# Kernel tuning notes

Measured on AMD Instinct MI355X. Metric: run time of the kernel, lower is better.

The kernel has to match this reference:

```python
import jax, jax.numpy as jnp
import numpy as np

N_QUBITS = 10
N_LAYERS = 2
B = 4096
D_IN = 512
D_OUT = 256


def _apply_1q(state, gate, wire, n):
    # state: (B, 2**n) complex64; gate: (2,2) shared or (B,2,2) batched
    b = state.shape[0]
    left, right = 2 ** wire, 2 ** (n - wire - 1)
    s = state.reshape(b, left, 2, right)
    if gate.ndim == 3:
        s = jnp.einsum('bij,bljr->blir', gate, s)
    else:
        s = jnp.einsum('ij,bljr->blir', gate, s)
    return s.reshape(b, 2 ** n)


def _apply_cnot(state, c, t, n):
    # CNOT(control=c, target=t): flip target axis on the control=1 slice
    b = state.shape[0]
    a, d = (c, t) if c < t else (t, c)
    s = state.reshape(b, 2 ** a, 2, 2 ** (d - a - 1), 2, 2 ** (n - d - 1))
    if c < t:
        s = s.at[:, :, 1].set(jnp.flip(s[:, :, 1], axis=3))
    else:
        s = s.at[:, :, :, :, 1].set(jnp.flip(s[:, :, :, :, 1], axis=2))
    return s.reshape(b, 2 ** n)


def _quantum_circuit(angles, qweights):
    # AngleEmbedding (RX) + StronglyEntanglingLayers (Rot + ring CNOTs), expval(PauliZ_i)
    b, n = angles.shape
    n_layers = qweights.shape[0]
    state = jnp.zeros((b, 2 ** n), jnp.complex64).at[:, 0].set(1.0)
    # AngleEmbedding default rotation='X': RX(angle_i) on wire i
    half = 0.5 * angles
    cx = jnp.cos(half).astype(jnp.complex64)
    sx = ((-1j) * jnp.sin(half)).astype(jnp.complex64)
    for i in range(n):
        gate = jnp.stack([jnp.stack([cx[:, i], sx[:, i]], -1),
                          jnp.stack([sx[:, i], cx[:, i]], -1)], -2)  # (B,2,2)
        state = _apply_1q(state, gate, i, n)
    for l in range(n_layers):
        phi, theta, omega = qweights[l, :, 0], qweights[l, :, 1], qweights[l, :, 2]
        ct = jnp.cos(0.5 * theta).astype(jnp.complex64)
        st = jnp.sin(0.5 * theta).astype(jnp.complex64)
        epo = jnp.exp(-0.5j * (phi + omega)).astype(jnp.complex64)
        epm = jnp.exp(-0.5j * (phi - omega)).astype(jnp.complex64)
        # Rot(phi,theta,omega) = RZ(omega) RY(theta) RZ(phi)
        gates = jnp.stack([jnp.stack([epo * ct, -jnp.conj(epm) * st], -1),
                           jnp.stack([epm * st, jnp.conj(epo) * ct], -1)], -2)  # (n,2,2)
        for i in range(n):
            state = _apply_1q(state, gates[i], i, n)
        if n > 1:
            r = (l % (n - 1)) + 1  # default StronglyEntanglingLayers range
            for i in range(n):
                state = _apply_cnot(state, i, (i + r) % n, n)
    probs = state.real ** 2 + state.imag ** 2  # (B, 2**n)
    k = np.arange(2 ** n)
    # wire 0 is the most-significant bit; z_i = +1 for bit 0, -1 for bit 1
    zmat = (1 - 2 * ((k[None, :] >> (n - 1 - np.arange(n))[:, None]) & 1)).astype(np.float32)
    return probs @ zmat.T  # (B, n)


def setup_inputs() -> dict:
    key = jax.random.key(0)
    ks = jax.random.split(key, 6)
    x = jax.random.normal(ks[0], (B, D_IN), jnp.float32)
    W_in = jax.random.normal(ks[1], (D_IN, N_QUBITS), jnp.float32) / np.float32(np.sqrt(D_IN))
    b_in = jnp.zeros((N_QUBITS,), jnp.float32)
    qweights = jax.random.uniform(ks[2], (N_LAYERS, N_QUBITS, 3), jnp.float32, 0.0, 2.0 * np.pi)
    W1 = jax.random.normal(ks[3], (N_QUBITS, 64), jnp.float32) / np.float32(np.sqrt(N_QUBITS))
    b1 = jnp.zeros((64,), jnp.float32)
    W2 = jax.random.normal(ks[4], (64, D_OUT), jnp.float32) / np.float32(8.0)
    b2 = jnp.zeros((D_OUT,), jnp.float32)
    return {'x': x, 'W_in': W_in, 'b_in': b_in, 'qweights': qweights,
            'W1': W1, 'b1': b1, 'W2': W2, 'b2': b2}


def reference(x, W_in, b_in, qweights, W1, b1, W2, b2):
    angles = x @ W_in + b_in          # input projection -> rotation angles
    z = _quantum_circuit(angles, qweights)  # (B, n_qubits) PauliZ expvals
    h = jax.nn.relu(z @ W1 + b1)
    return jnp.tanh(h @ W2 + b2)
```

## Files before the change

kernel.cpp:

```cpp
#include <hip/hip_runtime.h>
#include <math.h>

#define NQ 10

__device__ __forceinline__ void write_term(int u, const float abc[NQ][3],
                                           uint2* __restrict__ terms) {
    const int lane = u & 255, s = u >> 8;
    int q = -1, g0 = 0;
    if      (lane < 32)  { q = 8; g0 = 0;   }
    else if (lane < 64)  { q = 9; g0 = 32;  }
    else if (lane < 96)  { q = 0; g0 = 64;  }
    else if (lane < 128) { q = 1; g0 = 96;  }
    else if (lane < 160) { q = 6; g0 = 128; }
    else if (lane < 192) { q = 7; g0 = 160; }
    else if (lane < 200) { q = 4; g0 = 192; }
    else if (lane < 208) { q = 5; g0 = 200; }
    else if (lane < 216) { q = 2; g0 = 208; }
    else if (lane < 224) { q = 3; g0 = 216; }
    if (q < 0) { terms[u] = make_uint2(0u, 0u); return; }
    const int tau = (lane - g0) * 8 + s;

    int m = 1 << q;
    for (int ii = NQ - 1; ii >= 0; --ii) {
        int tt = (ii + 2) % NQ;
        if ((m >> tt) & 1) m ^= 1 << ii;
    }
    const int Lp = __popc(m);
    int cnt = 1;
    for (int k = 0; k < Lp; ++k) cnt *= 3;
    if (tau >= cnt) { terms[u] = make_uint2(0u, 0u); return; }

    int rem = tau;
    unsigned xm = 0, zm = 0;
    float coef = 1.f;
    for (int i = 0; i < NQ; ++i) {
        if ((m >> i) & 1) {
            int d = rem % 3; rem /= 3;
            coef *= abc[i][d];
            if (d == 0)      { xm |= 1u << i; }
            else if (d == 1) { xm |= 1u << i; zm |= 1u << i; }
            else             { zm |= 1u << i; }
        }
    }
    unsigned sgn = 0;
    for (int i = NQ - 1; i >= 0; --i) {
        int c = i, tt = (i + 1) % NQ;
        unsigned xc = (xm >> c) & 1u, zt = (zm >> tt) & 1u;
        unsigned xt = (xm >> tt) & 1u, zc = (zm >> c) & 1u;
        sgn ^= xc & zt & (xt ^ zc ^ 1u);
        xm ^= xc << tt;
        zm ^= zt << c;
    }
    if (sgn) coef = -coef;

    unsigned nib = 0;
    for (int p = 0; p < 5; ++p) {
        unsigned c0 = ((xm >> (2 * p)) & 1u) | (((zm >> (2 * p)) & 1u) << 1);
        unsigned c1 = ((xm >> (2 * p + 1)) & 1u) | (((zm >> (2 * p + 1)) & 1u) << 1);
        nib |= (c0 | (c1 << 2)) << (4 * p);
    }
    terms[u] = make_uint2(nib, __float_as_uint(coef));
}

__global__ __launch_bounds__(256) void qse_setup(const float* __restrict__ qw,
                                                 uint2* __restrict__ terms,
                                                 float* __restrict__ Rmat) {
    __shared__ float abc[NQ][3];
    const int t = threadIdx.x;
    const int b = blockIdx.x;
    if (t < NQ) {
        if (b == 0) {
            float phi = qw[t * 3 + 0], th = qw[t * 3 + 1], om = qw[t * 3 + 2];
            float st_, ct;  sincosf(0.5f * th, &st_, &ct);
            float spo, cpo; sincosf(0.5f * (phi + om), &spo, &cpo);
            float spm, cpm; sincosf(0.5f * (phi - om), &spm, &cpm);
            Rmat[t * 8 + 0] =  cpo * ct;  Rmat[t * 8 + 1] = -spo * ct;
            Rmat[t * 8 + 2] = -cpm * st_; Rmat[t * 8 + 3] = -spm * st_;
            Rmat[t * 8 + 4] =  cpm * st_; Rmat[t * 8 + 5] = -spm * st_;
            Rmat[t * 8 + 6] =  cpo * ct;  Rmat[t * 8 + 7] =  spo * ct;
        }
        {
            float phi = qw[30 + t * 3 + 0], th = qw[30 + t * 3 + 1], om = qw[30 + t * 3 + 2];
            float st_, ct;  sincosf(0.5f * th, &st_, &ct);
            float spo, cpo; sincosf(0.5f * (phi + om), &spo, &cpo);
            float spm, cpm; sincosf(0.5f * (phi - om), &spm, &cpm);
            float2 G00 = make_float2(cpo * ct, -spo * ct);
            float2 G01 = make_float2(-cpm * st_, -spm * st_);
            float2 G10 = make_float2(cpm * st_, -spm * st_);
            float2 G11 = make_float2(cpo * ct, spo * ct);
            float re = G00.x * G01.x + G00.y * G01.y - (G10.x * G11.x + G10.y * G11.y);
            float im = G00.x * G01.y - G00.y * G01.x - (G10.x * G11.y - G10.y * G11.x);
            float A00 = G00.x * G00.x + G00.y * G00.y - (G10.x * G10.x + G10.y * G10.y);
            float A11 = G01.x * G01.x + G01.y * G01.y - (G11.x * G11.x + G11.y * G11.y);
            abc[t][0] = re;
            abc[t][1] = -im;
            abc[t][2] = 0.5f * (A00 - A11);
        }
    }
    __syncthreads();
    write_term(b * 256 + t, abc, terms);
}

__device__ __forceinline__ float fast_tanh(float v) {
    float e = __expf(2.f * v);
    return 1.f - 2.f / (e + 1.f);
}

__global__ __launch_bounds__(256) void qse_mega(
    const float* __restrict__ x,
    const float* __restrict__ W_in,
    const float* __restrict__ b_in,
    const float* __restrict__ W1,
    const float* __restrict__ b1,
    const float* __restrict__ W2,
    const float* __restrict__ b2,
    const uint2* __restrict__ terms,
    const float* __restrict__ Rmat,
    float* __restrict__ out)
{
    __shared__ float angsh[4][NQ];
    __shared__ float E2d[4][5][32];
    __shared__ float zsh[4][NQ];
    __shared__ float hsh[4][64];

    const int t = threadIdx.x;
    const int lane = t & 63;
    const int wv = t >> 6;
    const int row0 = blockIdx.x * 4;

    uint2 tm[8];
    #pragma unroll
    for (int s = 0; s < 8; ++s) tm[s] = terms[s * 256 + t];

    {
        float acc[NQ];
        #pragma unroll
        for (int q = 0; q < NQ; ++q) acc[q] = 0.f;
        const float4* xr4 = (const float4*)(x + (size_t)(row0 + wv) * 512);
        #pragma unroll
        for (int k = 0; k < 2; ++k) {
            const int j4 = lane + 64 * k;
            const float4 xv = xr4[j4];
            const float* wr = W_in + (4 * j4) * NQ;
            #pragma unroll
            for (int h = 0; h < 5; ++h) {
                float2 w2 = ((const float2*)wr)[h];
                acc[2*h]   = fmaf(xv.x, w2.x, acc[2*h]);
                acc[2*h+1] = fmaf(xv.x, w2.y, acc[2*h+1]);
            }
            #pragma unroll
            for (int h = 0; h < 5; ++h) {
                float2 w2 = ((const float2*)(wr + NQ))[h];
                acc[2*h]   = fmaf(xv.y, w2.x, acc[2*h]);
                acc[2*h+1] = fmaf(xv.y, w2.y, acc[2*h+1]);
            }
            #pragma unroll
            for (int h = 0; h < 5; ++h) {
                float2 w2 = ((const float2*)(wr + 2 * NQ))[h];
                acc[2*h]   = fmaf(xv.z, w2.x, acc[2*h]);
                acc[2*h+1] = fmaf(xv.z, w2.y, acc[2*h+1]);
            }
            #pragma unroll
            for (int h = 0; h < 5; ++h) {
                float2 w2 = ((const float2*)(wr + 3 * NQ))[h];
                acc[2*h]   = fmaf(xv.w, w2.x, acc[2*h]);
                acc[2*h+1] = fmaf(xv.w, w2.y, acc[2*h+1]);
            }
        }
        #pragma unroll
        for (int off = 32; off > 0; off >>= 1) {
            #pragma unroll
            for (int q = 0; q < NQ; ++q) acc[q] += __shfl_xor(acc[q], off);
        }
        if (lane == 0) {
            #pragma unroll
            for (int q = 0; q < NQ; ++q) angsh[wv][q] = acc[q] + b_in[q];
        }
    }
    __syncthreads();

    if (t < 80) {
        const int rr = t / 20, rem = t % 20, p = rem >> 2, c1 = rem & 3;
        const int i0 = 2 * p, i1 = i0 + 1;
        float a0 = angsh[rr][i0];
        float a1 = angsh[rr][i1];
        float s0, c0f, s1, c1f;
        sincosf(0.5f * a0, &s0, &c0f);
        sincosf(0.5f * a1, &s1, &c1f);
        const float* Rp0 = Rmat + i0 * 8;
        const float* Rp1 = Rmat + i1 * 8;
        float2 u0 = make_float2(fmaf(Rp0[0], c0f, s0 * Rp0[3]), fmaf(Rp0[1], c0f, -s0 * Rp0[2]));
        float2 u1 = make_float2(fmaf(Rp0[4], c0f, s0 * Rp0[7]), fmaf(Rp0[5], c0f, -s0 * Rp0[6]));
        float ex0 = 2.f * (u0.x * u1.x + u0.y * u1.y);
        float ey0 = 2.f * (u0.x * u1.y - u0.y * u1.x);
        float ez0 = u0.x * u0.x + u0.y * u0.y - u1.x * u1.x - u1.y * u1.y;
        float2 v0 = make_float2(fmaf(Rp1[0], c1f, s1 * Rp1[3]), fmaf(Rp1[1], c1f, -s1 * Rp1[2]));
        float2 v1 = make_float2(fmaf(Rp1[4], c1f, s1 * Rp1[7]), fmaf(Rp1[5], c1f, -s1 * Rp1[6]));
        float ex1 = 2.f * (v0.x * v1.x + v0.y * v1.y);
        float ey1 = 2.f * (v0.x * v1.y - v0.y * v1.x);
        float ez1 = v0.x * v0.x + v0.y * v0.y - v1.x * v1.x - v1.y * v1.y;
        float e1 = (c1 == 0) ? 1.f : (c1 == 1) ? ex1 : (c1 == 2) ? ez1 : ey1;
        float e0arr[4] = {1.f, ex0, ez0, ey0};
        #pragma unroll
        for (int cc = 0; cc < 4; ++cc) {
            float v = e0arr[cc] * e1;
            int idx = cc | (c1 << 2);
            E2d[rr][p][2 * idx]     = v;
            E2d[rr][p][2 * idx + 1] = v;
        }
    }
    __syncthreads();

    float accR[4] = {0.f, 0.f, 0.f, 0.f};
    {
        const float* E2p = &E2d[0][0][0] + (t & 1);
        #pragma unroll
        for (int s = 0; s < 8; ++s) {
            const float cf = __uint_as_float(tm[s].y);
            const unsigned nib = tm[s].x;
            #pragma unroll
            for (int rr = 0; rr < 4; ++rr) {
                float pr = cf;
                #pragma unroll
                for (int p = 0; p < 5; ++p)
                    pr *= E2p[(rr * 5 + p) * 32 + 2 * ((nib >> (4 * p)) & 15u)];
                accR[rr] += pr;
            }
        }
    }
    #pragma unroll
    for (int rr = 0; rr < 4; ++rr) {
        accR[rr] += __shfl_xor(accR[rr], 1);
        accR[rr] += __shfl_xor(accR[rr], 2);
        accR[rr] += __shfl_xor(accR[rr], 4);
    }
    if (t < 192) {
        #pragma unroll
        for (int rr = 0; rr < 4; ++rr) {
            accR[rr] += __shfl_xor(accR[rr], 8);
            accR[rr] += __shfl_xor(accR[rr], 16);
        }
    }
    {
        int qx = -1;
        if      (t == 0)   qx = 8;
        else if (t == 32)  qx = 9;
        else if (t == 64)  qx = 0;
        else if (t == 96)  qx = 1;
        else if (t == 128) qx = 6;
        else if (t == 160) qx = 7;
        else if (t == 192) qx = 4;
        else if (t == 200) qx = 5;
        else if (t == 208) qx = 2;
        else if (t == 216) qx = 3;
        if (qx >= 0) {
            #pragma unroll
            for (int rr = 0; rr < 4; ++rr) zsh[rr][qx] = accR[rr];
        }
    }
    __syncthreads();

    {
        const int rr = t >> 6, c = t & 63;
        float a = b1[c];
        #pragma unroll
        for (int i = 0; i < NQ; ++i) a = fmaf(zsh[rr][i], W1[i * 64 + c], a);
        hsh[rr][c] = fmaxf(a, 0.f);
    }
    __syncthreads();

    {
        float oacc[4];
        const float bb = b2[t];
        #pragma unroll
        for (int rr = 0; rr < 4; ++rr) oacc[rr] = bb;
        for (int j4 = 0; j4 < 16; ++j4) {
            const float w0 = W2[(4 * j4 + 0) * 256 + t];
            const float w1 = W2[(4 * j4 + 1) * 256 + t];
            const float w2 = W2[(4 * j4 + 2) * 256 + t];
            const float w3 = W2[(4 * j4 + 3) * 256 + t];
            #pragma unroll
            for (int rr = 0; rr < 4; ++rr) {
                float4 hv = *(const float4*)&hsh[rr][4 * j4];
                oacc[rr] = fmaf(hv.x, w0, oacc[rr]);
                oacc[rr] = fmaf(hv.y, w1, oacc[rr]);
                oacc[rr] = fmaf(hv.z, w2, oacc[rr]);
                oacc[rr] = fmaf(hv.w, w3, oacc[rr]);
            }
        }
        #pragma unroll
        for (int rr = 0; rr < 4; ++rr)
            out[(size_t)(row0 + rr) * 256 + t] = fast_tanh(oacc[rr]);
    }
}

extern "C" void kernel_launch(void* const* d_in, const int* in_sizes, int n_in,
                              void* d_out, int out_size, void* d_ws, size_t ws_size,
                              hipStream_t stream) {
    const float* x    = (const float*)d_in[0];
    const float* W_in = (const float*)d_in[1];
    const float* b_in = (const float*)d_in[2];
    const float* qw   = (const float*)d_in[3];
    const float* W1   = (const float*)d_in[4];
    const float* b1   = (const float*)d_in[5];
    const float* W2   = (const float*)d_in[6];
    const float* b2   = (const float*)d_in[7];
    float* out = (float*)d_out;

    uint2* terms = (uint2*)d_ws;
    float* Rmat  = (float*)((char*)d_ws + 16384);

    qse_setup<<<8, 256, 0, stream>>>(qw, terms, Rmat);
    qse_mega<<<1024, 256, 0, stream>>>(x, W_in, b_in, W1, b1, W2, b2,
                                       (const uint2*)terms, (const float*)Rmat, out);
}
```

Measured before the change: 87.52 us.

## Precompute 4-qubit expectation tables and trim per-wave term slots

Replaces the five per-pair lookups per Pauli term with two 256-entry 4-qubit product tables plus one pair table, built in shared memory per row. This cuts shared loads and multiplies in the term-summation loop. It also sizes the number of term slots per wave to the actual term counts, so waves 1-3 skip the empty iterations. In exchange it adds a table-building pass and an extra barrier, and the non-uniform per-wave loop counts could cost some register or branch overhead.

New measurement: 84.92 us. 3.0% less time.

```diff
diff --git a/kernel.cpp b/kernel.cpp
--- a/kernel.cpp
+++ b/kernel.cpp
@@ -6,6 +6,8 @@
 __device__ __forceinline__ void write_term(int u, const float abc[NQ][3],
                                            uint2* __restrict__ terms) {
     const int lane = u & 255, s = u >> 8;
+    const int wvv = lane >> 6;
+    const int nsl = (wvv == 0) ? 8 : ((wvv == 3) ? 4 : 3);
     int q = -1, g0 = 0;
     if      (lane < 32)  { q = 8; g0 = 0;   }
     else if (lane < 64)  { q = 9; g0 = 32;  }
@@ -17,8 +19,8 @@
     else if (lane < 208) { q = 5; g0 = 200; }
     else if (lane < 216) { q = 2; g0 = 208; }
     else if (lane < 224) { q = 3; g0 = 216; }
-    if (q < 0) { terms[u] = make_uint2(0u, 0u); return; }
-    const int tau = (lane - g0) * 8 + s;
+    if (q < 0 || s >= nsl) { terms[u] = make_uint2(0u, 0u); return; }
+    const int tau = (lane - g0) * nsl + s;
 
     int m = 1 << q;
     for (int ii = NQ - 1; ii >= 0; --ii) {
@@ -53,13 +55,12 @@
     }
     if (sgn) coef = -coef;
 
-    unsigned nib = 0;
-    for (int p = 0; p < 5; ++p) {
-        unsigned c0 = ((xm >> (2 * p)) & 1u) | (((zm >> (2 * p)) & 1u) << 1);
-        unsigned c1 = ((xm >> (2 * p + 1)) & 1u) | (((zm >> (2 * p + 1)) & 1u) << 1);
-        nib |= (c0 | (c1 << 2)) << (4 * p);
-    }
-    terms[u] = make_uint2(nib, __float_as_uint(coef));
+    unsigned w = 0;
+    for (int i = 0; i < NQ; ++i) {
+        unsigned code = ((xm >> i) & 1u) | (((zm >> i) & 1u) << 1);
+        w |= code << (2 * i);
+    }
+    terms[u] = make_uint2(w, __float_as_uint(coef));
 }
 
 __global__ __launch_bounds__(256) void qse_setup(const float* __restrict__ qw,
@@ -119,7 +120,9 @@
     float* __restrict__ out)
 {
     __shared__ float angsh[4][NQ];
-    __shared__ float E2d[4][5][32];
+    __shared__ float E2tmp[4][5][16];
+    __shared__ float E4d[4][2][256];
+    __shared__ float E2P[4][32];
     __shared__ float zsh[4][NQ];
     __shared__ float hsh[4][64];
 
@@ -127,10 +130,12 @@
     const int lane = t & 63;
     const int wv = t >> 6;
     const int row0 = blockIdx.x * 4;
+    const int nsl = (wv == 0) ? 8 : ((wv == 3) ? 4 : 3);
 
     uint2 tm[8];
     #pragma unroll
-    for (int s = 0; s < 8; ++s) tm[s] = terms[s * 256 + t];
+    for (int s = 0; s < 8; ++s)
+        tm[s] = (s < nsl) ? terms[s * 256 + t] : make_uint2(0u, 0u);
 
     {
         float acc[NQ];
@@ -205,26 +210,38 @@
         for (int cc = 0; cc < 4; ++cc) {
             float v = e0arr[cc] * e1;
             int idx = cc | (c1 << 2);
-            E2d[rr][p][2 * idx]     = v;
-            E2d[rr][p][2 * idx + 1] = v;
-        }
+            E2tmp[rr][p][idx] = v;
+            if (p == 4) {
+                E2P[rr][2 * idx]     = v;
+                E2P[rr][2 * idx + 1] = v;
+            }
+        }
+    }
+    __syncthreads();
+
+    #pragma unroll
+    for (int k = 0; k < 8; ++k) {
+        const int rr = k >> 1, qd = k & 1;
+        E4d[rr][qd][t] = E2tmp[rr][2 * qd][t & 15] * E2tmp[rr][2 * qd + 1][t >> 4];
     }
     __syncthreads();
 
     float accR[4] = {0.f, 0.f, 0.f, 0.f};
     {
-        const float* E2p = &E2d[0][0][0] + (t & 1);
+        const int par = t & 1;
         #pragma unroll
         for (int s = 0; s < 8; ++s) {
-            const float cf = __uint_as_float(tm[s].y);
-            const unsigned nib = tm[s].x;
-            #pragma unroll
-            for (int rr = 0; rr < 4; ++rr) {
-                float pr = cf;
+            if (s < nsl) {
+                const float cf = __uint_as_float(tm[s].y);
+                const unsigned w = tm[s].x;
+                const int i0 = w & 255, i1 = (w >> 8) & 255, ip = (w >> 16) & 15;
                 #pragma unroll
-                for (int p = 0; p < 5; ++p)
-                    pr *= E2p[(rr * 5 + p) * 32 + 2 * ((nib >> (4 * p)) & 15u)];
-                accR[rr] += pr;
+                for (int rr = 0; rr < 4; ++rr) {
+                    float pr = cf * E4d[rr][0][i0];
+                    pr *= E4d[rr][1][i1];
+                    pr *= E2P[rr][2 * ip + par];
+                    accR[rr] += pr;
+                }
             }
         }
     }
```
